# Kernel optimization log

Measured on AMD Instinct MI355X. Metric: run time of the kernel, lower is better.

## Reference

```python
import jax, jax.numpy as jnp
import numpy as np

D = 256; NH = 8; NL = 4; NP = 4; DH = D // NH; DFFN = 1024; NQ = 900; BS = 4
SPATIAL = ((92, 92), (46, 46), (23, 23), (12, 12))  # (H, W) per level
LEVEL_START = (0, 8464, 10580, 11109)
S = sum(h * w for h, w in SPATIAL)  # 11253


def _ln(x, g, b):
    m = jnp.mean(x, -1, keepdims=True)
    v = jnp.var(x, -1, keepdims=True)
    return (x - m) / jnp.sqrt(v + 1e-5) * g + b


def setup_inputs() -> dict:
    key = jax.random.key(0)
    ks = jax.random.split(key, 24)
    p = lambda k, s: 0.02 * jax.random.normal(k, s, jnp.float32)
    return {
        "tgt": jax.random.normal(ks[0], (NQ, BS, D), jnp.float32),
        "tgt_query_pos": jax.random.normal(ks[1], (NQ, BS, D), jnp.float32),
        "tgt_reference_points": jax.random.uniform(ks[2], (NQ, BS, NL, 2), jnp.float32),
        "memory": jax.random.normal(ks[3], (S, BS, D), jnp.float32),
        "memory_spatial_shapes": jnp.array(SPATIAL, jnp.int32),
        "memory_level_start_index": jnp.array(LEVEL_START, jnp.int32),
        "in_proj_w": p(ks[4], (3 * D, D)), "in_proj_b": p(ks[5], (3 * D,)),
        "out_proj_w": p(ks[6], (D, D)), "out_proj_b": p(ks[7], (D,)),
        "off_w": p(ks[8], (NH * NL * NP * 2, D)), "off_b": p(ks[9], (NH * NL * NP * 2,)),
        "aw_w": p(ks[10], (NH * NL * NP, D)), "aw_b": p(ks[11], (NH * NL * NP,)),
        "vproj_w": p(ks[12], (D, D)), "vproj_b": p(ks[13], (D,)),
        "oproj_w": p(ks[14], (D, D)), "oproj_b": p(ks[15], (D,)),
        "ln1_g": jnp.ones((D,), jnp.float32), "ln1_b": jnp.zeros((D,), jnp.float32),
        "ln2_g": jnp.ones((D,), jnp.float32), "ln2_b": jnp.zeros((D,), jnp.float32),
        "ln3_g": jnp.ones((D,), jnp.float32), "ln3_b": jnp.zeros((D,), jnp.float32),
        "lin1_w": p(ks[16], (DFFN, D)), "lin1_b": p(ks[17], (DFFN,)),
        "lin2_w": p(ks[18], (D, DFFN)), "lin2_b": p(ks[19], (D,)),
    }


def _self_attn(q, k, v, in_w, in_b, out_w, out_b):
    # q, k, v: (nq, bs, d) -- torch nn.MultiheadAttention, eval mode
    wq, wk, wv = jnp.split(in_w, 3, axis=0)
    bq, bk, bv = jnp.split(in_b, 3)
    qp = (q @ wq.T + bq).reshape(NQ, BS, NH, DH)
    kp = (k @ wk.T + bk).reshape(NQ, BS, NH, DH)
    vp = (v @ wv.T + bv).reshape(NQ, BS, NH, DH)
    s = jnp.einsum("qbhd,kbhd->bhqk", qp, kp) / jnp.sqrt(jnp.float32(DH))
    a = jax.nn.softmax(s, axis=-1)
    o = jnp.einsum("bhqk,kbhd->qbhd", a, vp).reshape(NQ, BS, D)
    return o @ out_w.T + out_b


def _msdeform(x, ref, mem, off_w, off_b, aw_w, aw_b, vproj_w, vproj_b, oproj_w, oproj_b):
    # x: (bs, nq, d); ref: (bs, nq, nl, 2) in [0,1]; mem: (bs, S, d)
    value = (mem @ vproj_w.T + vproj_b).reshape(BS, S, NH, DH)
    off = (x @ off_w.T + off_b).reshape(BS, NQ, NH, NL, NP, 2)
    aw = jax.nn.softmax((x @ aw_w.T + aw_b).reshape(BS, NQ, NH, NL * NP), axis=-1)
    aw = aw.reshape(BS, NQ, NH, NL, NP)
    # offset normalizer = (W, H) per level
    norm = jnp.array([[w, h] for (h, w) in SPATIAL], jnp.float32)
    loc = ref[:, :, None, :, None, :] + off / norm[None, None, None, :, None, :]
    out = jnp.zeros((BS, NH, NQ, DH), x.dtype)
    for l, (H, W) in enumerate(SPATIAL):
        s0 = LEVEL_START[l]
        v = value[:, s0:s0 + H * W].transpose(0, 2, 1, 3)  # (bs, nh, H*W, dh)
        g = loc[:, :, :, l].transpose(0, 2, 1, 3, 4)       # (bs, nh, nq, np, 2)
        # grid_sample align_corners=False, padding_mode='zeros'
        px = g[..., 0] * W - 0.5
        py = g[..., 1] * H - 0.5
        x0 = jnp.floor(px).astype(jnp.int32)
        y0 = jnp.floor(py).astype(jnp.int32)
        wx = px - x0
        wy = py - y0
        samp = jnp.zeros((BS, NH, NQ, NP, DH), x.dtype)
        for dx, dy, w in ((0, 0, (1 - wx) * (1 - wy)), (1, 0, wx * (1 - wy)),
                          (0, 1, (1 - wx) * wy), (1, 1, wx * wy)):
            xi = x0 + dx
            yi = y0 + dy
            valid = ((xi >= 0) & (xi < W) & (yi >= 0) & (yi < H)).astype(x.dtype)
            idx = (jnp.clip(yi, 0, H - 1) * W + jnp.clip(xi, 0, W - 1)).reshape(BS, NH, NQ * NP)
            gat = jnp.take_along_axis(v, idx[..., None], axis=2).reshape(BS, NH, NQ, NP, DH)
            samp = samp + (w * valid)[..., None] * gat
        a = aw[:, :, :, l].transpose(0, 2, 1, 3)  # (bs, nh, nq, np)
        out = out + (samp * a[..., None]).sum(axis=3)
    out = out.transpose(0, 2, 1, 3).reshape(BS, NQ, D)
    return out @ oproj_w.T + oproj_b


def reference(tgt, tgt_query_pos, tgt_reference_points, memory,
              memory_spatial_shapes, memory_level_start_index,
              in_proj_w, in_proj_b, out_proj_w, out_proj_b,
              off_w, off_b, aw_w, aw_b, vproj_w, vproj_b, oproj_w, oproj_b,
              ln1_g, ln1_b, ln2_g, ln2_b, ln3_g, ln3_b,
              lin1_w, lin1_b, lin2_w, lin2_b):
    # module_seq = ['sa', 'ca', 'ffn']; dropout inactive (eval)
    q = tgt + tgt_query_pos
    tgt2 = _self_attn(q, q, tgt, in_proj_w, in_proj_b, out_proj_w, out_proj_b)
    tgt = _ln(tgt + tgt2, ln2_g, ln2_b)
    x = (tgt + tgt_query_pos).transpose(1, 0, 2)
    ref = tgt_reference_points.transpose(1, 0, 2, 3)
    mem = memory.transpose(1, 0, 2)
    tgt2 = _msdeform(x, ref, mem, off_w, off_b, aw_w, aw_b,
                     vproj_w, vproj_b, oproj_w, oproj_b).transpose(1, 0, 2)
    tgt = _ln(tgt + tgt2, ln1_g, ln1_b)
    ff = jax.nn.relu(tgt @ lin1_w.T + lin1_b) @ lin2_w.T + lin2_b
    return _ln(tgt + ff, ln3_g, ln3_b)
```

## Files before the change

### kernel.cpp

```cpp
#include <hip/hip_runtime.h>
#include <math.h>

#define D_MODEL 256
#define NHEAD   8
#define NLVL    4
#define NPTS    4
#define DHEAD   32
#define DFFN    1024
#define NQ      900
#define BSZ     4
#define NROW    (NQ * BSZ)
#define S_TOT   11253
#define VROWS   (S_TOT * BSZ)
#define SASCALE 0.17677669529663687f

typedef __attribute__((ext_vector_type(8))) short short8;
typedef __attribute__((ext_vector_type(4))) float f32x4;
typedef unsigned short ushort_t;

static __device__ __forceinline__ unsigned f2bf1(float f) {
    unsigned u = __float_as_uint(f);
    return (u + 0x7FFFu + ((u >> 16) & 1u)) >> 16;
}
static __device__ __forceinline__ unsigned pack2bf(float x, float y) {
    return f2bf1(x) | (f2bf1(y) << 16);
}
static __device__ __forceinline__ float bf2f(ushort_t u) {
    return __uint_as_float(((unsigned)u) << 16);
}

#define GPAD 72

#if __has_builtin(__builtin_amdgcn_global_load_lds)
#define HAS_GLL 1
#endif

static __device__ __forceinline__ void stage_w16(const ushort_t* g, ushort_t* ldsbase, int lane)
{
#ifdef HAS_GLL
    __builtin_amdgcn_global_load_lds(
        (const __attribute__((address_space(1))) unsigned int*)g,
        (__attribute__((address_space(3))) unsigned int*)ldsbase, 16, 0, 0);
#else
    *(uint4*)(ldsbase + lane * 8) = *(const uint4*)g;
#endif
}

#define WB_IN   0
#define WB_VP   196608
#define WB_OUTP 262144
#define WB_OFF  327680
#define WB_AW   393216
#define WB_OP   425984
#define WB_L1   491520
#define WB_L2   753664
#define WB_TOT  1015808

__global__ __launch_bounds__(256) void cvt_weights(
    const float* __restrict__ w_in, const float* __restrict__ w_vp,
    const float* __restrict__ w_outp, const float* __restrict__ w_off,
    const float* __restrict__ w_aw, const float* __restrict__ w_op,
    const float* __restrict__ w_l1, const float* __restrict__ w_l2,
    ushort_t* __restrict__ dst)
{
    int b = blockIdx.x;
    const float* src;
    int dstoff;
    int kbits = 8;
    if (b < 96)       { src = w_in;   dstoff = WB_IN;   }
    else if (b < 128) { src = w_vp;   b -= 96;  dstoff = WB_VP;   }
    else if (b < 160) { src = w_outp; b -= 128; dstoff = WB_OUTP; }
    else if (b < 192) { src = w_off;  b -= 160; dstoff = WB_OFF;  }
    else if (b < 208) { src = w_aw;   b -= 192; dstoff = WB_AW;   }
    else if (b < 240) { src = w_op;   b -= 208; dstoff = WB_OP;   }
    else if (b < 368) { src = w_l1;   b -= 240; dstoff = WB_L1;   }
    else              { src = w_l2;   b -= 368; dstoff = WB_L2;   kbits = 10; }
    int i = (b * 256 + threadIdx.x) * 8;
    float4 f0 = *(const float4*)(src + i);
    float4 f1 = *(const float4*)(src + i + 4);
    uint4 u;
    u.x = pack2bf(f0.x, f0.y); u.y = pack2bf(f0.z, f0.w);
    u.z = pack2bf(f1.x, f1.y); u.w = pack2bf(f1.z, f1.w);
    int K = 1 << kbits;
    int n = i >> kbits;
    int k = i & (K - 1);
    int kswz = (k & ~63) | ((k & 63) ^ ((n & 7) << 3));
    *(uint4*)(dst + dstoff + (size_t)n * K + kswz) = u;
}

__global__ __launch_bounds__(256) void proj_fused(
    const float* __restrict__ tgt, const float* __restrict__ qpos,
    const ushort_t* __restrict__ in_wb, const float* __restrict__ in_b,
    const float* __restrict__ mem, const ushort_t* __restrict__ vp_wb,
    const float* __restrict__ vp_b,
    ushort_t* __restrict__ qkv16, ushort_t* __restrict__ value16)
{
    __shared__ ushort_t As[64 * GPAD];
    __shared__ ushort_t Ws[8704];

    const int t    = threadIdx.x;
    const int bid  = blockIdx.x;
    const int trow = t >> 2;
    const int tk   = (t & 3) << 4;
    const int wv   = t >> 6;
    const int ln   = t & 63;
    const int L    = ln & 15;
    const int quad = ln >> 4;
    const int swz  = (L & 7) << 3;
    const int lrow = ln >> 3;
    const int lchk = (ln & 7) << 3;

    if (bid < 684) {
        const int m0 = (bid % 57) * 64;
        const int n0 = (bid / 57) * 64;
        const bool addpos = (n0 < 512);
        const float oscale = (n0 < 256) ? SASCALE : 1.f;

        const int  mrow = m0 + trow;
        const bool mv   = (mrow < NROW);
        const float* arow = tgt  + (size_t)mrow * 256 + tk;
        const float* prow = qpos + (size_t)mrow * 256 + tk;

        f32x4 acc[4] = {{0.f,0.f,0.f,0.f},{0.f,0.f,0.f,0.f},
                        {0.f,0.f,0.f,0.f},{0.f,0.f,0.f,0.f}};

        for (int k0 = 0; k0 < 256; k0 += 64) {
#pragma unroll
            for (int j = 0; j < 2; ++j) {
                int r0 = (wv * 2 + j) * 8;
                const ushort_t* g = in_wb + (size_t)(n0 + r0 + lrow) * 256 + k0 + lchk;
                stage_w16(g, &Ws[r0 * 64], ln);
            }
            uint4 u0, u1;
            if (mv) {
                const float* ap = arow + k0;
                float4 a0 = *(const float4*)(ap + 0);
                float4 a1 = *(const float4*)(ap + 4);
                float4 a2 = *(const float4*)(ap + 8);
                float4 a3 = *(const float4*)(ap + 12);
                if (addpos) {
                    const float* pp = prow + k0;
                    float4 p0 = *(const float4*)(pp + 0);
                    float4 p1 = *(const float4*)(pp + 4);
                    float4 p2 = *(const float4*)(pp + 8);
                    float4 p3 = *(const float4*)(pp + 12);
                    a0.x += p0.x; a0.y += p0.y; a0.z += p0.z; a0.w += p0.w;
                    a1.x += p1.x; a1.y += p1.y; a1.z += p1.z; a1.w += p1.w;
                    a2.x += p2.x; a2.y += p2.y; a2.z += p2.z; a2.w += p2.w;
                    a3.x += p3.x; a3.y += p3.y; a3.z += p3.z; a3.w += p3.w;
                }
                u0.x = pack2bf(a0.x, a0.y); u0.y = pack2bf(a0.z, a0.w);
                u0.z = pack2bf(a1.x, a1.y); u0.w = pack2bf(a1.z, a1.w);
                u1.x = pack2bf(a2.x, a2.y); u1.y = pack2bf(a2.z, a2.w);
                u1.z = pack2bf(a3.x, a3.y); u1.w = pack2bf(a3.z, a3.w);
            } else {
                u0 = make_uint4(0u, 0u, 0u, 0u); u1 = u0;
            }
            *(uint4*)&As[trow * GPAD + tk + 0] = u0;
            *(uint4*)&As[trow * GPAD + tk + 8] = u1;
            __syncthreads();
#pragma unroll
            for (int kh = 0; kh < 2; ++kh) {
                short8 af = *(const short8*)&As[(wv * 16 + L) * GPAD + kh * 32 + quad * 8];
#pragma unroll
                for (int cb = 0; cb < 4; ++cb) {
                    short8 bf = *(const short8*)&Ws[(cb * 16 + L) * 64 + ((kh * 32 + quad * 8) ^ swz)];
                    acc[cb] = __builtin_amdgcn_mfma_f32_16x16x32_bf16(af, bf, acc[cb], 0, 0, 0);
                }
            }
            __syncthreads();
        }
#pragma unroll
        for (int cb = 0; cb < 4; ++cb) {
            int col = n0 + cb * 16 + L;
            float bv = in_b[col];
#pragma unroll
            for (int i = 0; i < 4; ++i) {
                int m = m0 + wv * 16 + quad * 4 + i;
                if (m < NROW)
                    qkv16[(size_t)m * 768 + col] = (ushort_t)f2bf1((acc[cb][i] + bv) * oscale);
            }
        }
    } else {
        const int vb = bid - 684;
        const int m0 = vb * 64;

        const int  mrow = m0 + trow;
        const bool mv   = (mrow < VROWS);
        const float* arow = mem + (size_t)mrow * 256 + tk;

        f32x4 acc[16];
#pragma unroll
        for (int i = 0; i < 16; ++i) acc[i] = (f32x4){0.f, 0.f, 0.f, 0.f};

        for (int k0 = 0; k0 < 256; k0 += 64) {
#pragma unroll
            for (int j = 0; j < 4; ++j) {
                int r0 = (wv * 4 + j) * 8;
                const ushort_t* g = vp_wb + (size_t)(r0 + lrow) * 256 + k0 + lchk;
                stage_w16(g, &Ws[r0 * 64], ln);
            }
            uint4 u0, u1;
            if (mv) {
                const float* ap = arow + k0;
                float4 a0 = *(const float4*)(ap + 0);
                float4 a1 = *(const float4*)(ap + 4);
                float4 a2 = *(const float4*)(ap + 8);
                float4 a3 = *(const float4*)(ap + 12);
                u0.x = pack2bf(a0.x, a0.y); u0.y = pack2bf(a0.z, a0.w);
                u0.z = pack2bf(a1.x, a1.y); u0.w = pack2bf(a1.z, a1.w);
                u1.x = pack2bf(a2.x, a2.y); u1.y = pack2bf(a2.z, a2.w);
                u1.z = pack2bf(a3.x, a3.y); u1.w = pack2bf(a3.z, a3.w);
            } else {
                u0 = make_uint4(0u, 0u, 0u, 0u); u1 = u0;
            }
            *(uint4*)&As[trow * GPAD + tk + 0] = u0;
            *(uint4*)&As[trow * GPAD + tk + 8] = u1;
            __syncthreads();
#pragma unroll
            for (int kh = 0; kh < 2; ++kh) {
                short8 af = *(const short8*)&As[(wv * 16 + L) * GPAD + kh * 32 + quad * 8];
#pragma unroll
                for (int cb = 0; cb < 8; ++cb) {
                    short8 bf = *(const short8*)&Ws[(cb * 16 + L) * 64 + ((kh * 32 + quad * 8) ^ swz)];
                    acc[cb] = __builtin_amdgcn_mfma_f32_16x16x32_bf16(af, bf, acc[cb], 0, 0, 0);
                }
            }
            __syncthreads();
#pragma unroll
            for (int j = 0; j < 4; ++j) {
                int r0 = (wv * 4 + j) * 8;
                const ushort_t* g = vp_wb + (size_t)(128 + r0 + lrow) * 256 + k0 + lchk;
                stage_w16(g, &Ws[r0 * 64], ln);
            }
            __syncthreads();
#pragma unroll
            for (int kh = 0; kh < 2; ++kh) {
                short8 af = *(const short8*)&As[(wv * 16 + L) * GPAD + kh * 32 + quad * 8];
#pragma unroll
                for (int cb = 0; cb < 8; ++cb) {
                    short8 bf = *(const short8*)&Ws[(cb * 16 + L) * 64 + ((kh * 32 + quad * 8) ^ swz)];
                    acc[8 + cb] = __builtin_amdgcn_mfma_f32_16x16x32_bf16(af, bf, acc[8 + cb], 0, 0, 0);
                }
            }
            __syncthreads();
        }

        ushort_t* Cs = Ws;
#pragma unroll
        for (int half = 0; half < 2; ++half) {
            if (half) __syncthreads();
#pragma unroll
            for (int cb = 0; cb < 8; ++cb) {
                int col = cb * 16 + L;
                float bv = vp_b[half * 128 + col];
#pragma unroll
                for (int i = 0; i < 4; ++i) {
                    int r = wv * 16 + quad * 4 + i;
                    Cs[r * 136 + col] = (ushort_t)f2bf1(acc[half * 8 + cb][i] + bv);
                }
            }
            __syncthreads();
            {
                int r  = t >> 2;
                int ch = (t & 3) * 32;
                int m  = m0 + r;
                if (m < VROWS) {
                    const ushort_t* src = &Cs[r * 136 + ch];
                    uint4* dst = (uint4*)(value16 + (size_t)m * 256 + half * 128 + ch);
#pragma unroll
                    for (int j = 0; j < 4; ++j)
                        dst[j] = *(const uint4*)(src + j * 8);
                }
            }
        }
    }
}

__global__ __launch_bounds__(256) void sa_flash16(
    const ushort_t* __restrict__ qkv, ushort_t* __restrict__ attn_out)
{
    __shared__ ushort_t Ks[2 * 2080];
    __shared__ ushort_t Vt[2 * 2304];
    __shared__ ushort_t Ps[4 * 1152];

    const int t    = threadIdx.x;
    const int q0   = blockIdx.x * 64;
    const int b    = blockIdx.y & 3;
    const int h    = blockIdx.y >> 2;
    const int wv   = t >> 6;
    const int ln   = t & 63;
    const int L    = ln & 15;
    const int quad = ln >> 4;

    union { uint4 u; short8 s; } qu;
    qu.u = make_uint4(0u, 0u, 0u, 0u);
    {
        int q = q0 + wv * 16 + L;
        if (q < NQ)
            qu.u = *(const uint4*)(qkv + ((size_t)q * 4 + b) * 768 + h * 32 + quad * 8);
    }
    const short8 qf = qu.s;

    float mrun = -1e30f, lrun = 0.f;
    f32x4 oacc[2] = {{0.f,0.f,0.f,0.f},{0.f,0.f,0.f,0.f}};

    const int skey = t >> 2;
    const int sdg  = t & 3;

    uint4 ku, vu;
    auto kv_load = [&](int k0) {
        int kg = k0 + skey;
        ku = make_uint4(0u, 0u, 0u, 0u);
        vu = make_uint4(0u, 0u, 0u, 0u);
        if (kg < NQ) {
            const ushort_t* base = qkv + ((size_t)kg * 4 + b) * 768 + 256 + h * 32 + sdg * 8;
            ku = *(const uint4*)base;
            vu = *(const uint4*)(base + 256);
        }
    };

    kv_load(0);
    int it = 0;
    for (int k0 = 0; k0 < NQ; k0 += 64, it ^= 1) {
        *(uint4*)&Ks[it * 2080 + sdg * 520 + skey * 8] = ku;
        {
            ushort_t* vp = &Vt[it * 2304 + sdg * 8 * 72 + skey];
            vp[0 * 72] = (ushort_t)(vu.x & 0xffffu);
            vp[1 * 72] = (ushort_t)(vu.x >> 16);
            vp[2 * 72] = (ushort_t)(vu.y & 0xffffu);
            vp[3 * 72] = (ushort_t)(vu.y >> 16);
            vp[4 * 72] = (ushort_t)(vu.z & 0xffffu);
            vp[5 * 72] = (ushort_t)(vu.z >> 16);
            vp[6 * 72] = (ushort_t)(vu.w & 0xffffu);
            vp[7 * 72] = (ushort_t)(vu.w >> 16);
        }
        __syncthreads();
        if (k0 + 64 < NQ) kv_load(k0 + 64);

        f32x4 sacc[4] = {{0.f,0.f,0.f,0.f},{0.f,0.f,0.f,0.f},
                         {0.f,0.f,0.f,0.f},{0.f,0.f,0.f,0.f}};
#pragma unroll
        for (int cb = 0; cb < 4; ++cb) {
            short8 kf = *(const short8*)&Ks[it * 2080 + quad * 520 + (cb * 16 + L) * 8];
            sacc[cb] = __builtin_amdgcn_mfma_f32_16x16x32_bf16(kf, qf, sacc[cb], 0, 0, 0);
        }
        if (k0 + 64 > NQ) {
#pragma unroll
            for (int cb = 0; cb < 4; ++cb)
#pragma unroll
                for (int i = 0; i < 4; ++i)
                    if (k0 + cb * 16 + quad * 4 + i >= NQ) sacc[cb][i] = -1e30f;
        }

        float ml = -1e30f;
#pragma unroll
        for (int cb = 0; cb < 4; ++cb)
#pragma unroll
            for (int i = 0; i < 4; ++i) ml = fmaxf(ml, sacc[cb][i]);
        ml = fmaxf(ml, __shfl_xor(ml, 16, 64));
        ml = fmaxf(ml, __shfl_xor(ml, 32, 64));
        float mnew  = fmaxf(mrun, ml);
        float alpha = __expf(mrun - mnew);
        float p[16];
        float rs = 0.f;
#pragma unroll
        for (int cb = 0; cb < 4; ++cb)
#pragma unroll
            for (int i = 0; i < 4; ++i) {
                float e = __expf(sacc[cb][i] - mnew);
                p[cb * 4 + i] = e;
                rs += e;
            }
        rs += __shfl_xor(rs, 16, 64);
        rs += __shfl_xor(rs, 32, 64);
        lrun = lrun * alpha + rs;
        mrun = mnew;

        {
            ushort_t* pw = &Ps[wv * 1152 + L * 72];
#pragma unroll
            for (int cb = 0; cb < 4; ++cb) {
                uint2 u;
                u.x = pack2bf(p[cb * 4 + 0], p[cb * 4 + 1]);
                u.y = pack2bf(p[cb * 4 + 2], p[cb * 4 + 3]);
                *(uint2*)&pw[cb * 16 + quad * 4] = u;
            }
        }
#pragma unroll
        for (int i = 0; i < 4; ++i) {
            float ai = __shfl(alpha, quad * 4 + i, 64);
            oacc[0][i] *= ai;
            oacc[1][i] *= ai;
        }
        __syncthreads();

#pragma unroll
        for (int ks = 0; ks < 2; ++ks) {
            short8 pf = *(const short8*)&Ps[wv * 1152 + L * 72 + ks * 32 + quad * 8];
#pragma unroll
            for (int db = 0; db < 2; ++db) {
                short8 vf = *(const short8*)&Vt[it * 2304 + (db * 16 + L) * 72 + ks * 32 + quad * 8];
                oacc[db] = __builtin_amdgcn_mfma_f32_16x16x32_bf16(pf, vf, oacc[db], 0, 0, 0);
            }
        }
    }

#pragma unroll
    for (int i = 0; i < 4; ++i) {
        float lq = __shfl(lrun, quad * 4 + i, 64);
        float li = 1.f / lq;
        int q = q0 + wv * 16 + quad * 4 + i;
        if (q < NQ) {
            ushort_t* op = attn_out + ((size_t)q * 4 + b) * 256 + h * 32 + L;
            op[0]  = (ushort_t)f2bf1(oacc[0][i] * li);
            op[16] = (ushort_t)f2bf1(oacc[1][i] * li);
        }
    }
}

__global__ __launch_bounds__(256) void fused_ca(
    const ushort_t* __restrict__ att16,
    const float* __restrict__ tgt, const float* __restrict__ qpos,
    const ushort_t* __restrict__ outp_wb, const float* __restrict__ outp_b,
    const float* __restrict__ ln2g, const float* __restrict__ ln2b,
    const ushort_t* __restrict__ off_wb, const float* __restrict__ off_b,
    const ushort_t* __restrict__ aw_wb, const float* __restrict__ aw_b,
    const float* __restrict__ refp,
    float* __restrict__ tgt_a, float* __restrict__ px_g,
    float* __restrict__ py_g, float* __restrict__ aw_g)
{
    __shared__ ushort_t Ws[256 * 64];
    __shared__ ushort_t As[16 * GPAD];
    __shared__ ushort_t xca_s[16 * 264];
    __shared__ float    aws[16 * 128];
    __shared__ float    sS[4][16], s2S[4][16];

    const int t    = threadIdx.x;
    const int m0   = blockIdx.x * 16;
    const int wv   = t >> 6;
    const int ln   = t & 63;
    const int L    = ln & 15;
    const int quad = ln >> 4;
    const int swz  = (L & 7) << 3;
    const int lrow = ln >> 3;
    const int lchk = (ln & 7) << 3;
    const int rloc = quad * 4;

    {
        f32x4 acc[4] = {{0.f,0.f,0.f,0.f},{0.f,0.f,0.f,0.f},
                        {0.f,0.f,0.f,0.f},{0.f,0.f,0.f,0.f}};
        for (int k0 = 0; k0 < 256; k0 += 64) {
#pragma unroll
            for (int j = 0; j < 8; ++j) {
                int r0 = (wv * 8 + j) * 8;
                const ushort_t* g = outp_wb + (size_t)(r0 + lrow) * 256 + k0 + lchk;
                stage_w16(g, &Ws[r0 * 64], ln);
            }
            if (t < 128) {
                int r = t >> 3, seg = (t & 7) * 8;
                uint4 a = *(const uint4*)(att16 + (size_t)(m0 + r) * 256 + k0 + seg);
                *(uint4*)&As[r * GPAD + seg] = a;
            }
            __syncthreads();
#pragma unroll
            for (int kh = 0; kh < 2; ++kh) {
                short8 af = *(const short8*)&As[L * GPAD + kh * 32 + quad * 8];
#pragma unroll
                for (int cb = 0; cb < 4; ++cb) {
                    short8 bf = *(const short8*)&Ws[(wv * 64 + cb * 16 + L) * 64 + ((kh * 32 + quad * 8) ^ swz)];
                    acc[cb] = __builtin_amdgcn_mfma_f32_16x16x32_bf16(af, bf, acc[cb], 0, 0, 0);
                }
            }
            __syncthreads();
        }
        float s[4] = {0.f,0.f,0.f,0.f}, s2v[4] = {0.f,0.f,0.f,0.f};
#pragma unroll
        for (int cb = 0; cb < 4; ++cb) {
            int col = wv * 64 + cb * 16 + L;
            float bv = outp_b[col];
#pragma unroll
            for (int i = 0; i < 4; ++i) {
                float xv = acc[cb][i] + bv + tgt[(size_t)(m0 + rloc + i) * 256 + col];
                acc[cb][i] = xv;
                s[i] += xv; s2v[i] += xv * xv;
            }
        }
#pragma unroll
        for (int off = 1; off < 16; off <<= 1)
#pragma unroll
            for (int i = 0; i < 4; ++i) {
                s[i]   += __shfl_xor(s[i],   off, 64);
                s2v[i] += __shfl_xor(s2v[i], off, 64);
            }
        if (L == 0)
#pragma unroll
            for (int i = 0; i < 4; ++i) { sS[wv][rloc + i] = s[i]; s2S[wv][rloc + i] = s2v[i]; }
        __syncthreads();
        float mean[4], rstd[4];
#pragma unroll
        for (int i = 0; i < 4; ++i) {
            float St  = sS[0][rloc+i] + sS[1][rloc+i] + sS[2][rloc+i] + sS[3][rloc+i];
            float S2t = s2S[0][rloc+i] + s2S[1][rloc+i] + s2S[2][rloc+i] + s2S[3][rloc+i];
            mean[i] = St * (1.f / 256.f);
            float var = S2t * (1.f / 256.f) - mean[i] * mean[i];
            rstd[i] = rsqrtf(var + 1e-5f);
        }
#pragma unroll
        for (int cb = 0; cb < 4; ++cb) {
            int col = wv * 64 + cb * 16 + L;
            float gv = ln2g[col], bt = ln2b[col];
#pragma unroll
            for (int i = 0; i < 4; ++i) {
                float y = (acc[cb][i] - mean[i]) * rstd[i] * gv + bt;
                tgt_a[(size_t)(m0 + rloc + i) * 256 + col] = y;
                xca_s[(rloc + i) * 264 + col] =
                    (ushort_t)f2bf1(y + qpos[(size_t)(m0 + rloc + i) * 256 + col]);
            }
        }
        __syncthreads();
    }

    {
        f32x4 acc[4] = {{0.f,0.f,0.f,0.f},{0.f,0.f,0.f,0.f},
                        {0.f,0.f,0.f,0.f},{0.f,0.f,0.f,0.f}};
        for (int k0 = 0; k0 < 256; k0 += 64) {
#pragma unroll
            for (int j = 0; j < 8; ++j) {
                int r0 = (wv * 8 + j) * 8;
                const ushort_t* g = off_wb + (size_t)(r0 + lrow) * 256 + k0 + lchk;
                stage_w16(g, &Ws[r0 * 64], ln);
            }
            __syncthreads();
#pragma unroll
            for (int kh = 0; kh < 2; ++kh) {
                short8 af = *(const short8*)&xca_s[L * 264 + k0 + kh * 32 + quad * 8];
#pragma unroll
                for (int cb = 0; cb < 4; ++cb) {
                    short8 bf = *(const short8*)&Ws[(wv * 64 + cb * 16 + L) * 64 + ((kh * 32 + quad * 8) ^ swz)];
                    acc[cb] = __builtin_amdgcn_mfma_f32_16x16x32_bf16(af, bf, acc[cb], 0, 0, 0);
                }
            }
            __syncthreads();
        }
        const float dims[4] = {92.f, 46.f, 23.f, 12.f};
#pragma unroll
        for (int cb = 0; cb < 4; ++cb) {
            int col = wv * 64 + cb * 16 + L;
            float bv = off_b[col];
            int hh = col >> 5, lp = (col & 31) >> 1, isY = col & 1;
            int l = lp >> 2;
            float dim = dims[l];
            float* dst = isY ? py_g : px_g;
#pragma unroll
            for (int i = 0; i < 4; ++i) {
                int row = m0 + rloc + i;
                float ref = refp[((size_t)row * 4 + l) * 2 + isY];
                dst[(size_t)row * 128 + hh * 16 + lp] = ref * dim + (acc[cb][i] + bv) - 0.5f;
            }
        }
    }

    {
        f32x4 acc2[2] = {{0.f,0.f,0.f,0.f},{0.f,0.f,0.f,0.f}};
        for (int k0 = 0; k0 < 256; k0 += 64) {
#pragma unroll
            for (int j = 0; j < 4; ++j) {
                int r0 = (wv * 4 + j) * 8;
                const ushort_t* g = aw_wb + (size_t)(r0 + lrow) * 256 + k0 + lchk;
                stage_w16(g, &Ws[r0 * 64], ln);
            }
            __syncthreads();
#pragma unroll
            for (int kh = 0; kh < 2; ++kh) {
                short8 af = *(const short8*)&xca_s[L * 264 + k0 + kh * 32 + quad * 8];
#pragma unroll
                for (int cb = 0; cb < 2; ++cb) {
                    short8 bf = *(const short8*)&Ws[(wv * 32 + cb * 16 + L) * 64 + ((kh * 32 + quad * 8) ^ swz)];
                    acc2[cb] = __builtin_amdgcn_mfma_f32_16x16x32_bf16(af, bf, acc2[cb], 0, 0, 0);
                }
            }
            __syncthreads();
        }
#pragma unroll
        for (int cb = 0; cb < 2; ++cb) {
            int col = wv * 32 + cb * 16 + L;
            float bv = aw_b[col];
#pragma unroll
            for (int i = 0; i < 4; ++i)
                aws[(rloc + i) * 128 + col] = acc2[cb][i] + bv;
        }
        __syncthreads();
    }

    if (t < 128) {
        int r = t >> 3, hh = t & 7;
        float v[16];
        float m = -1e30f;
#pragma unroll
        for (int j = 0; j < 16; ++j) { v[j] = aws[r * 128 + hh * 16 + j]; m = fmaxf(m, v[j]); }
        float ssum = 0.f;
#pragma unroll
        for (int j = 0; j < 16; ++j) { v[j] = __expf(v[j] - m); ssum += v[j]; }
        float inv = 1.f / ssum;
#pragma unroll
        for (int j = 0; j < 16; ++j)
            aw_g[(size_t)(m0 + r) * 128 + hh * 16 + j] = v[j] * inv;
    }
}

__global__ __launch_bounds__(256) void msdeform4(
    const float* __restrict__ px_g, const float* __restrict__ py_g,
    const float* __restrict__ aw_g, const ushort_t* __restrict__ value16,
    ushort_t* __restrict__ out)
{
    const int t   = threadIdx.x;
    const int row = blockIdx.x * 4 + (t >> 6);
    const int ln  = t & 63;
    const int h   = ln >> 3;
    const int d   = (ln & 7) * 4;
    const int b   = row & 3;

    const int HsI[4] = {92, 46, 23, 12};
    const int S0_[4] = {0, 8464, 10580, 11109};

    const ushort_t* vb = value16 + (size_t)b * 256 + h * 32 + d;
    const float* pxr = px_g + (size_t)row * 128 + h * 16;
    const float* pyr = py_g + (size_t)row * 128 + h * 16;
    const float* awr = aw_g + (size_t)row * 128 + h * 16;

    float a0 = 0.f, a1 = 0.f, a2 = 0.f, a3 = 0.f;
#pragma unroll
    for (int l = 0; l < 4; ++l) {
        const int H = HsI[l], W = HsI[l], base = S0_[l];
#pragma unroll
        for (int p = 0; p < 4; ++p) {
            const int lp = l * 4 + p;
            float px = pxr[lp], py = pyr[lp], aw = awr[lp];
            float x0f = floorf(px), y0f = floorf(py);
            int x0 = (int)x0f, y0 = (int)y0f;
            float wx = px - x0f, wy = py - y0f;
            float s0 = 0.f, s1 = 0.f, s2 = 0.f, s3 = 0.f;
#pragma unroll
            for (int dy = 0; dy < 2; ++dy) {
#pragma unroll
                for (int dx = 0; dx < 2; ++dx) {
                    int xi = x0 + dx, yi = y0 + dy;
                    float flag = (xi >= 0 && xi < W && yi >= 0 && yi < H) ? 1.f : 0.f;
                    int xc = xi < 0 ? 0 : (xi >= W ? W - 1 : xi);
                    int yc = yi < 0 ? 0 : (yi >= H ? H - 1 : yi);
                    float wgt = (dx ? wx : 1.f - wx) * (dy ? wy : 1.f - wy) * flag;
                    uint2 gv = *(const uint2*)(vb + (size_t)(base + yc * W + xc) * 1024);
                    s0 = fmaf(wgt, bf2f((ushort_t)(gv.x & 0xffffu)), s0);
                    s1 = fmaf(wgt, bf2f((ushort_t)(gv.x >> 16)), s1);
                    s2 = fmaf(wgt, bf2f((ushort_t)(gv.y & 0xffffu)), s2);
                    s3 = fmaf(wgt, bf2f((ushort_t)(gv.y >> 16)), s3);
                }
            }
            a0 = fmaf(aw, s0, a0);
            a1 = fmaf(aw, s1, a1);
            a2 = fmaf(aw, s2, a2);
            a3 = fmaf(aw, s3, a3);
        }
    }
    uint2 u;
    u.x = pack2bf(a0, a1);
    u.y = pack2bf(a2, a3);
    *(uint2*)(out + (size_t)row * 256 + h * 32 + d) = u;
}

__global__ __launch_bounds__(256) void ffn_fused(
    const ushort_t* __restrict__ att2_16,
    const float* __restrict__ tgt_a,
    const ushort_t* __restrict__ op_wb, const float* __restrict__ op_b,
    const float* __restrict__ ln1g, const float* __restrict__ ln1b,
    const ushort_t* __restrict__ l1_wb, const float* __restrict__ l1b,
    const ushort_t* __restrict__ l2_wb, const float* __restrict__ l2b,
    const float* __restrict__ ln3g, const float* __restrict__ ln3b,
    float* __restrict__ out)
{
    __shared__ ushort_t Ws[256 * 64];
    __shared__ ushort_t A1[16 * 264];
    __shared__ ushort_t hc[16 * 264];
    __shared__ float    sS[4][16], s2S[4][16];

    const int t    = threadIdx.x;
    const int m0   = blockIdx.x * 16;
    const int wv   = t >> 6;
    const int ln   = t & 63;
    const int L    = ln & 15;
    const int quad = ln >> 4;
    const int swz  = (L & 7) << 3;
    const int lrow = ln >> 3;
    const int lchk = (ln & 7) << 3;
    const int rloc = quad * 4;

#pragma unroll
    for (int jj = 0; jj < 2; ++jj) {
        int c = t * 2 + jj;
        int r = c >> 5, s = (c & 31) * 8;
        *(uint4*)&hc[r * 264 + s] = *(const uint4*)(att2_16 + (size_t)(m0 + r) * 256 + s);
    }

    f32x4 resid[4];

    {
        f32x4 acc[4] = {{0.f,0.f,0.f,0.f},{0.f,0.f,0.f,0.f},
                        {0.f,0.f,0.f,0.f},{0.f,0.f,0.f,0.f}};
        for (int k0 = 0; k0 < 256; k0 += 64) {
#pragma unroll
            for (int j = 0; j < 8; ++j) {
                int r0 = (wv * 8 + j) * 8;
                const ushort_t* g = op_wb + (size_t)(r0 + lrow) * 256 + k0 + lchk;
                stage_w16(g, &Ws[r0 * 64], ln);
            }
            __syncthreads();
#pragma unroll
            for (int kh = 0; kh < 2; ++kh) {
                short8 af = *(const short8*)&hc[L * 264 + k0 + kh * 32 + quad * 8];
#pragma unroll
                for (int cb = 0; cb < 4; ++cb) {
                    short8 bf = *(const short8*)&Ws[(wv * 64 + cb * 16 + L) * 64 + ((kh * 32 + quad * 8) ^ swz)];
                    acc[cb] = __builtin_amdgcn_mfma_f32_16x16x32_bf16(af, bf, acc[cb], 0, 0, 0);
                }
            }
            __syncthreads();
        }
        float s[4] = {0.f,0.f,0.f,0.f}, s2v[4] = {0.f,0.f,0.f,0.f};
#pragma unroll
        for (int cb = 0; cb < 4; ++cb) {
            int col = wv * 64 + cb * 16 + L;
            float bv = op_b[col];
#pragma unroll
            for (int i = 0; i < 4; ++i) {
                float xv = acc[cb][i] + bv + tgt_a[(size_t)(m0 + rloc + i) * 256 + col];
                acc[cb][i] = xv;
                s[i] += xv; s2v[i] += xv * xv;
            }
        }
#pragma unroll
        for (int off = 1; off < 16; off <<= 1)
#pragma unroll
            for (int i = 0; i < 4; ++i) {
                s[i]   += __shfl_xor(s[i],   off, 64);
                s2v[i] += __shfl_xor(s2v[i], off, 64);
            }
        if (L == 0)
#pragma unroll
            for (int i = 0; i < 4; ++i) { sS[wv][rloc + i] = s[i]; s2S[wv][rloc + i] = s2v[i]; }
        __syncthreads();
        float mean[4], rstd[4];
#pragma unroll
        for (int i = 0; i < 4; ++i) {
            float St  = sS[0][rloc+i] + sS[1][rloc+i] + sS[2][rloc+i] + sS[3][rloc+i];
            float S2t = s2S[0][rloc+i] + s2S[1][rloc+i] + s2S[2][rloc+i] + s2S[3][rloc+i];
            mean[i] = St * (1.f / 256.f);
            float var = S2t * (1.f / 256.f) - mean[i] * mean[i];
            rstd[i] = rsqrtf(var + 1e-5f);
        }
#pragma unroll
        for (int cb = 0; cb < 4; ++cb) {
            int col = wv * 64 + cb * 16 + L;
            float gv = ln1g[col], bt = ln1b[col];
#pragma unroll
            for (int i = 0; i < 4; ++i) {
                float y = (acc[cb][i] - mean[i]) * rstd[i] * gv + bt;
                resid[cb][i] = y;
                A1[(rloc + i) * 264 + col] = (ushort_t)f2bf1(y);
            }
        }
        __syncthreads();
    }

    f32x4 accf[4] = {{0.f,0.f,0.f,0.f},{0.f,0.f,0.f,0.f},
                     {0.f,0.f,0.f,0.f},{0.f,0.f,0.f,0.f}};
    for (int c = 0; c < 4; ++c) {
        f32x4 acch[4] = {{0.f,0.f,0.f,0.f},{0.f,0.f,0.f,0.f},
                         {0.f,0.f,0.f,0.f},{0.f,0.f,0.f,0.f}};
        for (int k0 = 0; k0 < 256; k0 += 64) {
#pragma unroll
            for (int j = 0; j < 8; ++j) {
                int r0 = (wv * 8 + j) * 8;
                const ushort_t* g = l1_wb + (size_t)(c * 256 + r0 + lrow) * 256 + k0 + lchk;
                stage_w16(g, &Ws[r0 * 64], ln);
            }
            __syncthreads();
#pragma unroll
            for (int kh = 0; kh < 2; ++kh) {
                short8 af = *(const short8*)&A1[L * 264 + k0 + kh * 32 + quad * 8];
#pragma unroll
                for (int cb = 0; cb < 4; ++cb) {
                    short8 bf = *(const short8*)&Ws[(wv * 64 + cb * 16 + L) * 64 + ((kh * 32 + quad * 8) ^ swz)];
                    acch[cb] = __builtin_amdgcn_mfma_f32_16x16x32_bf16(af, bf, acch[cb], 0, 0, 0);
                }
            }
            __syncthreads();
        }
#pragma unroll
        for (int cb = 0; cb < 4; ++cb) {
            int colc = wv * 64 + cb * 16 + L;
            float bv = l1b[c * 256 + colc];
#pragma unroll
            for (int i = 0; i < 4; ++i)
                hc[(rloc + i) * 264 + colc] = (ushort_t)f2bf1(fmaxf(acch[cb][i] + bv, 0.f));
        }
        __syncthreads();
        for (int k0 = 0; k0 < 256; k0 += 64) {
#pragma unroll
            for (int j = 0; j < 8; ++j) {
                int r0 = (wv * 8 + j) * 8;
                const ushort_t* g = l2_wb + (size_t)(r0 + lrow) * 1024 + c * 256 + k0 + lchk;
                stage_w16(g, &Ws[r0 * 64], ln);
            }
            __syncthreads();
#pragma unroll
            for (int kh = 0; kh < 2; ++kh) {
                short8 af = *(const short8*)&hc[L * 264 + k0 + kh * 32 + quad * 8];
#pragma unroll
                for (int cb = 0; cb < 4; ++cb) {
                    short8 bf = *(const short8*)&Ws[(wv * 64 + cb * 16 + L) * 64 + ((kh * 32 + quad * 8) ^ swz)];
                    accf[cb] = __builtin_amdgcn_mfma_f32_16x16x32_bf16(af, bf, accf[cb], 0, 0, 0);
                }
            }
            __syncthreads();
        }
    }

    {
        float s[4] = {0.f,0.f,0.f,0.f}, s2v[4] = {0.f,0.f,0.f,0.f};
#pragma unroll
        for (int cb = 0; cb < 4; ++cb) {
            int col = wv * 64 + cb * 16 + L;
            float bv = l2b[col];
#pragma unroll
            for (int i = 0; i < 4; ++i) {
                float xv = accf[cb][i] + bv + resid[cb][i];
                accf[cb][i] = xv;
                s[i] += xv; s2v[i] += xv * xv;
            }
        }
#pragma unroll
        for (int off = 1; off < 16; off <<= 1)
#pragma unroll
            for (int i = 0; i < 4; ++i) {
                s[i]   += __shfl_xor(s[i],   off, 64);
                s2v[i] += __shfl_xor(s2v[i], off, 64);
            }
        if (L == 0)
#pragma unroll
            for (int i = 0; i < 4; ++i) { sS[wv][rloc + i] = s[i]; s2S[wv][rloc + i] = s2v[i]; }
        __syncthreads();
        float mean[4], rstd[4];
#pragma unroll
        for (int i = 0; i < 4; ++i) {
            float St  = sS[0][rloc+i] + sS[1][rloc+i] + sS[2][rloc+i] + sS[3][rloc+i];
            float S2t = s2S[0][rloc+i] + s2S[1][rloc+i] + s2S[2][rloc+i] + s2S[3][rloc+i];
            mean[i] = St * (1.f / 256.f);
            float var = S2t * (1.f / 256.f) - mean[i] * mean[i];
            rstd[i] = rsqrtf(var + 1e-5f);
        }
#pragma unroll
        for (int cb = 0; cb < 4; ++cb) {
            int col = wv * 64 + cb * 16 + L;
            float gv = ln3g[col], bt = ln3b[col];
#pragma unroll
            for (int i = 0; i < 4; ++i) {
                float y = (accf[cb][i] - mean[i]) * rstd[i] * gv + bt;
                out[(size_t)(m0 + rloc + i) * 256 + col] = y;
            }
        }
    }
}

extern "C" void kernel_launch(void* const* d_in, const int* in_sizes, int n_in,
                              void* d_out, int out_size, void* d_ws, size_t ws_size,
                              hipStream_t stream)
{
    const float* tgt    = (const float*)d_in[0];
    const float* qpos   = (const float*)d_in[1];
    const float* refp   = (const float*)d_in[2];
    const float* mem    = (const float*)d_in[3];
    const float* in_w   = (const float*)d_in[6];
    const float* in_b   = (const float*)d_in[7];
    const float* outp_w = (const float*)d_in[8];
    const float* outp_b = (const float*)d_in[9];
    const float* off_w  = (const float*)d_in[10];
    const float* off_b  = (const float*)d_in[11];
    const float* aw_w   = (const float*)d_in[12];
    const float* aw_b   = (const float*)d_in[13];
    const float* vp_w   = (const float*)d_in[14];
    const float* vp_b   = (const float*)d_in[15];
    const float* op_w   = (const float*)d_in[16];
    const float* op_b   = (const float*)d_in[17];
    const float* ln1g   = (const float*)d_in[18];
    const float* ln1b   = (const float*)d_in[19];
    const float* ln2g   = (const float*)d_in[20];
    const float* ln2b   = (const float*)d_in[21];
    const float* ln3g   = (const float*)d_in[22];
    const float* ln3b   = (const float*)d_in[23];
    const float* l1w    = (const float*)d_in[24];
    const float* l1b    = (const float*)d_in[25];
    const float* l2w    = (const float*)d_in[26];
    const float* l2b    = (const float*)d_in[27];
    float* out = (float*)d_out;
    float* ws  = (float*)d_ws;

    ushort_t* qkv16    = (ushort_t*)ws;
    ushort_t* att16    = (ushort_t*)(ws + 691200);
    float*    tgt_a    = ws + 1843200;
    float*    px_g     = ws + 2995200;
    float*    py_g     = ws + 3456000;
    float*    aw_g     = ws + 3916800;
    ushort_t* att2_16  = (ushort_t*)(ws + 4377600);
    ushort_t* value16  = (ushort_t*)(ws + 5760000);
    ushort_t* wb       = (ushort_t*)(ws + 13364736);

    const ushort_t* in_wb   = wb + WB_IN;
    const ushort_t* vp_wb   = wb + WB_VP;
    const ushort_t* outp_wb = wb + WB_OUTP;
    const ushort_t* off_wb  = wb + WB_OFF;
    const ushort_t* aw_wb   = wb + WB_AW;
    const ushort_t* op_wb   = wb + WB_OP;
    const ushort_t* l1_wb   = wb + WB_L1;
    const ushort_t* l2_wb   = wb + WB_L2;

    dim3 b256(256);

    hipLaunchKernelGGL(cvt_weights, dim3(496), b256, 0, stream,
                       in_w, vp_w, outp_w, off_w, aw_w, op_w, l1w, l2w, wb);
    hipLaunchKernelGGL(proj_fused, dim3(1388), b256, 0, stream,
                       tgt, qpos, in_wb, in_b, mem, vp_wb, vp_b, qkv16, value16);
    hipLaunchKernelGGL(sa_flash16, dim3(15, 32), b256, 0, stream, qkv16, att16);
    hipLaunchKernelGGL(fused_ca, dim3(225), b256, 0, stream,
                       att16, tgt, qpos, outp_wb, outp_b, ln2g, ln2b,
                       off_wb, off_b, aw_wb, aw_b, refp,
                       tgt_a, px_g, py_g, aw_g);
    hipLaunchKernelGGL(msdeform4, dim3(900), b256, 0, stream,
                       px_g, py_g, aw_g, value16, att2_16);
    hipLaunchKernelGGL(ffn_fused, dim3(225), b256, 0, stream,
                       att2_16, tgt_a, op_wb, op_b, ln1g, ln1b,
                       l1_wb, l1b, l2_wb, l2b, ln3g, ln3b, out);
}
```

Baseline: 255.2 us.

## Pre-convert activations to bf16, double-buffer weights, widen fused kernels to 512 threads

The weight-conversion kernel now also converts tgt and tgt+qpos into swizzled bf16 buffers, so the QKV projection can stage its A tiles directly with global_load_lds instead of converting fp32 per tile. The value projection stages all 256 weight rows at once, removing a second staging pass and one barrier per k-step. fused_ca and ffn_fused move to 512 threads with double-buffered weight tiles in LDS, prefetching the next k-slice or the next GEMM's first slice while the current one computes, which halves the barriers per step. The cost is extra workspace traffic for the bf16 activation copies, more LDS per block, and a single resident block per CU for the fused kernels.

```diff
diff --git a/kernel.cpp b/kernel.cpp
--- a/kernel.cpp
+++ b/kernel.cpp
@@ -10,6 +10,7 @@
 #define NQ      900
 #define BSZ     4
 #define NROW    (NQ * BSZ)
+#define NROWP   3648
 #define S_TOT   11253
 #define VROWS   (S_TOT * BSZ)
 #define SASCALE 0.17677669529663687f
@@ -28,8 +29,6 @@
 static __device__ __forceinline__ float bf2f(ushort_t u) {
     return __uint_as_float(((unsigned)u) << 16);
 }
-
-#define GPAD 72
 
 #if __has_builtin(__builtin_amdgcn_global_load_lds)
 #define HAS_GLL 1
@@ -61,47 +60,73 @@
     const float* __restrict__ w_outp, const float* __restrict__ w_off,
     const float* __restrict__ w_aw, const float* __restrict__ w_op,
     const float* __restrict__ w_l1, const float* __restrict__ w_l2,
-    ushort_t* __restrict__ dst)
+    ushort_t* __restrict__ dst,
+    const float* __restrict__ tgt, const float* __restrict__ qpos,
+    ushort_t* __restrict__ tgt16, ushort_t* __restrict__ tq16)
 {
     int b = blockIdx.x;
-    const float* src;
-    int dstoff;
-    int kbits = 8;
-    if (b < 96)       { src = w_in;   dstoff = WB_IN;   }
-    else if (b < 128) { src = w_vp;   b -= 96;  dstoff = WB_VP;   }
-    else if (b < 160) { src = w_outp; b -= 128; dstoff = WB_OUTP; }
-    else if (b < 192) { src = w_off;  b -= 160; dstoff = WB_OFF;  }
-    else if (b < 208) { src = w_aw;   b -= 192; dstoff = WB_AW;   }
-    else if (b < 240) { src = w_op;   b -= 208; dstoff = WB_OP;   }
-    else if (b < 368) { src = w_l1;   b -= 240; dstoff = WB_L1;   }
-    else              { src = w_l2;   b -= 368; dstoff = WB_L2;   kbits = 10; }
-    int i = (b * 256 + threadIdx.x) * 8;
-    float4 f0 = *(const float4*)(src + i);
-    float4 f1 = *(const float4*)(src + i + 4);
-    uint4 u;
-    u.x = pack2bf(f0.x, f0.y); u.y = pack2bf(f0.z, f0.w);
-    u.z = pack2bf(f1.x, f1.y); u.w = pack2bf(f1.z, f1.w);
-    int K = 1 << kbits;
-    int n = i >> kbits;
-    int k = i & (K - 1);
-    int kswz = (k & ~63) | ((k & 63) ^ ((n & 7) << 3));
-    *(uint4*)(dst + dstoff + (size_t)n * K + kswz) = u;
+    if (b < 496) {
+        const float* src;
+        int dstoff;
+        int kbits = 8;
+        if (b < 96)       { src = w_in;   dstoff = WB_IN;   }
+        else if (b < 128) { src = w_vp;   b -= 96;  dstoff = WB_VP;   }
+        else if (b < 160) { src = w_outp; b -= 128; dstoff = WB_OUTP; }
+        else if (b < 192) { src = w_off;  b -= 160; dstoff = WB_OFF;  }
+        else if (b < 208) { src = w_aw;   b -= 192; dstoff = WB_AW;   }
+        else if (b < 240) { src = w_op;   b -= 208; dstoff = WB_OP;   }
+        else if (b < 368) { src = w_l1;   b -= 240; dstoff = WB_L1;   }
+        else              { src = w_l2;   b -= 368; dstoff = WB_L2;   kbits = 10; }
+        int i = (b * 256 + threadIdx.x) * 8;
+        float4 f0 = *(const float4*)(src + i);
+        float4 f1 = *(const float4*)(src + i + 4);
+        uint4 u;
+        u.x = pack2bf(f0.x, f0.y); u.y = pack2bf(f0.z, f0.w);
+        u.z = pack2bf(f1.x, f1.y); u.w = pack2bf(f1.z, f1.w);
+        int K = 1 << kbits;
+        int n = i >> kbits;
+        int k = i & (K - 1);
+        int kswz = (k & ~63) | ((k & 63) ^ ((n & 7) << 3));
+        *(uint4*)(dst + dstoff + (size_t)n * K + kswz) = u;
+    } else {
+        int bb = b - 496;
+        ushort_t* dbuf = tgt16;
+        bool addq = false;
+        if (bb >= 456) { bb -= 456; dbuf = tq16; addq = true; }
+        int i = bb * 2048 + threadIdx.x * 8;
+        int row = i >> 8, k = i & 255;
+        uint4 u = make_uint4(0u, 0u, 0u, 0u);
+        if (row < NROW) {
+            const float* sp = tgt + (size_t)row * 256 + k;
+            float4 f0 = *(const float4*)(sp + 0);
+            float4 f1 = *(const float4*)(sp + 4);
+            if (addq) {
+                const float* qp = qpos + (size_t)row * 256 + k;
+                float4 q0 = *(const float4*)(qp + 0);
+                float4 q1 = *(const float4*)(qp + 4);
+                f0.x += q0.x; f0.y += q0.y; f0.z += q0.z; f0.w += q0.w;
+                f1.x += q1.x; f1.y += q1.y; f1.z += q1.z; f1.w += q1.w;
+            }
+            u.x = pack2bf(f0.x, f0.y); u.y = pack2bf(f0.z, f0.w);
+            u.z = pack2bf(f1.x, f1.y); u.w = pack2bf(f1.z, f1.w);
+        }
+        int kswz = (k & ~63) | ((k & 63) ^ ((row & 7) << 3));
+        *(uint4*)(dbuf + (size_t)row * 256 + kswz) = u;
+    }
 }
 
 __global__ __launch_bounds__(256) void proj_fused(
-    const float* __restrict__ tgt, const float* __restrict__ qpos,
+    const ushort_t* __restrict__ tq16, const ushort_t* __restrict__ tgt16,
     const ushort_t* __restrict__ in_wb, const float* __restrict__ in_b,
     const float* __restrict__ mem, const ushort_t* __restrict__ vp_wb,
     const float* __restrict__ vp_b,
     ushort_t* __restrict__ qkv16, ushort_t* __restrict__ value16)
 {
-    __shared__ ushort_t As[64 * GPAD];
-    __shared__ ushort_t Ws[8704];
+    __shared__ ushort_t As[64 * 64];
+    __shared__ ushort_t Ws[256 * 64];
 
     const int t    = threadIdx.x;
     const int bid  = blockIdx.x;
-    const int trow = t >> 2;
-    const int tk   = (t & 3) << 4;
     const int wv   = t >> 6;
     const int ln   = t & 63;
     const int L    = ln & 15;
@@ -113,13 +138,8 @@
     if (bid < 684) {
         const int m0 = (bid % 57) * 64;
         const int n0 = (bid / 57) * 64;
-        const bool addpos = (n0 < 512);
         const float oscale = (n0 < 256) ? SASCALE : 1.f;
-
-        const int  mrow = m0 + trow;
-        const bool mv   = (mrow < NROW);
-        const float* arow = tgt  + (size_t)mrow * 256 + tk;
-        const float* prow = qpos + (size_t)mrow * 256 + tk;
+        const ushort_t* Ab = (n0 < 512) ? tq16 : tgt16;
 
         f32x4 acc[4] = {{0.f,0.f,0.f,0.f},{0.f,0.f,0.f,0.f},
                         {0.f,0.f,0.f,0.f},{0.f,0.f,0.f,0.f}};
@@ -128,43 +148,17 @@
 #pragma unroll
             for (int j = 0; j < 2; ++j) {
                 int r0 = (wv * 2 + j) * 8;
-                const ushort_t* g = in_wb + (size_t)(n0 + r0 + lrow) * 256 + k0 + lchk;
-                stage_w16(g, &Ws[r0 * 64], ln);
-            }
-            uint4 u0, u1;
-            if (mv) {
-                const float* ap = arow + k0;
-                float4 a0 = *(const float4*)(ap + 0);
-                float4 a1 = *(const float4*)(ap + 4);
-                float4 a2 = *(const float4*)(ap + 8);
-                float4 a3 = *(const float4*)(ap + 12);
-                if (addpos) {
-                    const float* pp = prow + k0;
-                    float4 p0 = *(const float4*)(pp + 0);
-                    float4 p1 = *(const float4*)(pp + 4);
-                    float4 p2 = *(const float4*)(pp + 8);
-                    float4 p3 = *(const float4*)(pp + 12);
-                    a0.x += p0.x; a0.y += p0.y; a0.z += p0.z; a0.w += p0.w;
-                    a1.x += p1.x; a1.y += p1.y; a1.z += p1.z; a1.w += p1.w;
-                    a2.x += p2.x; a2.y += p2.y; a2.z += p2.z; a2.w += p2.w;
-                    a3.x += p3.x; a3.y += p3.y; a3.z += p3.z; a3.w += p3.w;
-                }
-                u0.x = pack2bf(a0.x, a0.y); u0.y = pack2bf(a0.z, a0.w);
-                u0.z = pack2bf(a1.x, a1.y); u0.w = pack2bf(a1.z, a1.w);
-                u1.x = pack2bf(a2.x, a2.y); u1.y = pack2bf(a2.z, a2.w);
-                u1.z = pack2bf(a3.x, a3.y); u1.w = pack2bf(a3.z, a3.w);
-            } else {
-                u0 = make_uint4(0u, 0u, 0u, 0u); u1 = u0;
-            }
-            *(uint4*)&As[trow * GPAD + tk + 0] = u0;
-            *(uint4*)&As[trow * GPAD + tk + 8] = u1;
+                stage_w16(Ab + (size_t)(m0 + r0 + lrow) * 256 + k0 + lchk, &As[r0 * 64], ln);
+                stage_w16(in_wb + (size_t)(n0 + r0 + lrow) * 256 + k0 + lchk, &Ws[r0 * 64], ln);
+            }
             __syncthreads();
 #pragma unroll
             for (int kh = 0; kh < 2; ++kh) {
-                short8 af = *(const short8*)&As[(wv * 16 + L) * GPAD + kh * 32 + quad * 8];
+                int ko = (kh * 32 + quad * 8) ^ swz;
+                short8 af = *(const short8*)&As[(wv * 16 + L) * 64 + ko];
 #pragma unroll
                 for (int cb = 0; cb < 4; ++cb) {
-                    short8 bf = *(const short8*)&Ws[(cb * 16 + L) * 64 + ((kh * 32 + quad * 8) ^ swz)];
+                    short8 bf = *(const short8*)&Ws[(cb * 16 + L) * 64 + ko];
                     acc[cb] = __builtin_amdgcn_mfma_f32_16x16x32_bf16(af, bf, acc[cb], 0, 0, 0);
                 }
             }
@@ -184,6 +178,9 @@
     } else {
         const int vb = bid - 684;
         const int m0 = vb * 64;
+        const int trow = t >> 2;
+        const int tk   = (t & 3) << 4;
+        const int wsz  = (trow & 7) << 3;
 
         const int  mrow = m0 + trow;
         const bool mv   = (mrow < VROWS);
@@ -195,10 +192,9 @@
 
         for (int k0 = 0; k0 < 256; k0 += 64) {
 #pragma unroll
-            for (int j = 0; j < 4; ++j) {
-                int r0 = (wv * 4 + j) * 8;
-                const ushort_t* g = vp_wb + (size_t)(r0 + lrow) * 256 + k0 + lchk;
-                stage_w16(g, &Ws[r0 * 64], ln);
+            for (int j = 0; j < 8; ++j) {
+                int r0 = (wv * 8 + j) * 8;
+                stage_w16(vp_wb + (size_t)(r0 + lrow) * 256 + k0 + lchk, &Ws[r0 * 64], ln);
             }
             uint4 u0, u1;
             if (mv) {
@@ -214,33 +210,17 @@
             } else {
                 u0 = make_uint4(0u, 0u, 0u, 0u); u1 = u0;
             }
-            *(uint4*)&As[trow * GPAD + tk + 0] = u0;
-            *(uint4*)&As[trow * GPAD + tk + 8] = u1;
+            *(uint4*)&As[trow * 64 + (tk ^ wsz)]       = u0;
+            *(uint4*)&As[trow * 64 + ((tk + 8) ^ wsz)] = u1;
             __syncthreads();
 #pragma unroll
             for (int kh = 0; kh < 2; ++kh) {
-                short8 af = *(const short8*)&As[(wv * 16 + L) * GPAD + kh * 32 + quad * 8];
-#pragma unroll
-                for (int cb = 0; cb < 8; ++cb) {
-                    short8 bf = *(const short8*)&Ws[(cb * 16 + L) * 64 + ((kh * 32 + quad * 8) ^ swz)];
+                int ko = (kh * 32 + quad * 8) ^ swz;
+                short8 af = *(const short8*)&As[(wv * 16 + L) * 64 + ko];
+#pragma unroll
+                for (int cb = 0; cb < 16; ++cb) {
+                    short8 bf = *(const short8*)&Ws[(cb * 16 + L) * 64 + ko];
                     acc[cb] = __builtin_amdgcn_mfma_f32_16x16x32_bf16(af, bf, acc[cb], 0, 0, 0);
-                }
-            }
-            __syncthreads();
-#pragma unroll
-            for (int j = 0; j < 4; ++j) {
-                int r0 = (wv * 4 + j) * 8;
-                const ushort_t* g = vp_wb + (size_t)(128 + r0 + lrow) * 256 + k0 + lchk;
-                stage_w16(g, &Ws[r0 * 64], ln);
-            }
-            __syncthreads();
-#pragma unroll
-            for (int kh = 0; kh < 2; ++kh) {
-                short8 af = *(const short8*)&As[(wv * 16 + L) * GPAD + kh * 32 + quad * 8];
-#pragma unroll
-                for (int cb = 0; cb < 8; ++cb) {
-                    short8 bf = *(const short8*)&Ws[(cb * 16 + L) * 64 + ((kh * 32 + quad * 8) ^ swz)];
-                    acc[8 + cb] = __builtin_amdgcn_mfma_f32_16x16x32_bf16(af, bf, acc[8 + cb], 0, 0, 0);
                 }
             }
             __syncthreads();
@@ -419,7 +399,7 @@
     }
 }
 
-__global__ __launch_bounds__(256) void fused_ca(
+__global__ __launch_bounds__(512, 1) void fused_ca(
     const ushort_t* __restrict__ att16,
     const float* __restrict__ tgt, const float* __restrict__ qpos,
     const ushort_t* __restrict__ outp_wb, const float* __restrict__ outp_b,
@@ -430,11 +410,11 @@
     float* __restrict__ tgt_a, float* __restrict__ px_g,
     float* __restrict__ py_g, float* __restrict__ aw_g)
 {
-    __shared__ ushort_t Ws[256 * 64];
-    __shared__ ushort_t As[16 * GPAD];
+    __shared__ ushort_t Ws[2][256 * 64];
+    __shared__ ushort_t att_s[16 * 264];
     __shared__ ushort_t xca_s[16 * 264];
-    __shared__ float    aws[16 * 128];
-    __shared__ float    sS[4][16], s2S[4][16];
+    __shared__ float    aws_s[16 * 128];
+    __shared__ float    sS[8][16], s2S[8][16];
 
     const int t    = threadIdx.x;
     const int m0   = blockIdx.x * 16;
@@ -447,37 +427,54 @@
     const int lchk = (ln & 7) << 3;
     const int rloc = quad * 4;
 
+    auto stage4 = [&](const ushort_t* base, int buf) {
+#pragma unroll
+        for (int j = 0; j < 4; ++j) {
+            int r0 = (wv * 4 + j) * 8;
+            stage_w16(base + (size_t)(r0 + lrow) * 256 + lchk, &Ws[buf][r0 * 64], ln);
+        }
+    };
+    auto stage2 = [&](const ushort_t* base, int buf) {
+#pragma unroll
+        for (int j = 0; j < 2; ++j) {
+            int r0 = (wv * 2 + j) * 8;
+            stage_w16(base + (size_t)(r0 + lrow) * 256 + lchk, &Ws[buf][r0 * 64], ln);
+        }
+    };
+    auto mfma2 = [&](const ushort_t* A, int koff, int buf, f32x4* acc) {
+#pragma unroll
+        for (int kh = 0; kh < 2; ++kh) {
+            int ko = (kh * 32 + quad * 8) ^ swz;
+            short8 af = *(const short8*)&A[L * 264 + koff + kh * 32 + quad * 8];
+#pragma unroll
+            for (int cb = 0; cb < 2; ++cb) {
+                short8 bf = *(const short8*)&Ws[buf][(wv * 32 + cb * 16 + L) * 64 + ko];
+                acc[cb] = __builtin_amdgcn_mfma_f32_16x16x32_bf16(af, bf, acc[cb], 0, 0, 0);
+            }
+        }
+    };
+
     {
-        f32x4 acc[4] = {{0.f,0.f,0.f,0.f},{0.f,0.f,0.f,0.f},
-                        {0.f,0.f,0.f,0.f},{0.f,0.f,0.f,0.f}};
-        for (int k0 = 0; k0 < 256; k0 += 64) {
-#pragma unroll
-            for (int j = 0; j < 8; ++j) {
-                int r0 = (wv * 8 + j) * 8;
-                const ushort_t* g = outp_wb + (size_t)(r0 + lrow) * 256 + k0 + lchk;
-                stage_w16(g, &Ws[r0 * 64], ln);
-            }
-            if (t < 128) {
-                int r = t >> 3, seg = (t & 7) * 8;
-                uint4 a = *(const uint4*)(att16 + (size_t)(m0 + r) * 256 + k0 + seg);
-                *(uint4*)&As[r * GPAD + seg] = a;
-            }
-            __syncthreads();
-#pragma unroll
-            for (int kh = 0; kh < 2; ++kh) {
-                short8 af = *(const short8*)&As[L * GPAD + kh * 32 + quad * 8];
-#pragma unroll
-                for (int cb = 0; cb < 4; ++cb) {
-                    short8 bf = *(const short8*)&Ws[(wv * 64 + cb * 16 + L) * 64 + ((kh * 32 + quad * 8) ^ swz)];
-                    acc[cb] = __builtin_amdgcn_mfma_f32_16x16x32_bf16(af, bf, acc[cb], 0, 0, 0);
-                }
-            }
-            __syncthreads();
+        int r = t >> 5, s = (t & 31) * 8;
+        *(uint4*)&att_s[r * 264 + s] = *(const uint4*)(att16 + (size_t)(m0 + r) * 256 + s);
+    }
+    stage4(outp_wb, 0);
+    __syncthreads();
+    int cur = 0;
+
+    {
+        f32x4 acc[2] = {{0.f,0.f,0.f,0.f},{0.f,0.f,0.f,0.f}};
+        for (int k = 0; k < 4; ++k) {
+            if (k < 3) stage4(outp_wb + (k + 1) * 64, cur ^ 1);
+            else       stage4(off_wb, cur ^ 1);
+            mfma2(att_s, k * 64, cur, acc);
+            __syncthreads();
+            cur ^= 1;
         }
         float s[4] = {0.f,0.f,0.f,0.f}, s2v[4] = {0.f,0.f,0.f,0.f};
 #pragma unroll
-        for (int cb = 0; cb < 4; ++cb) {
-            int col = wv * 64 + cb * 16 + L;
+        for (int cb = 0; cb < 2; ++cb) {
+            int col = wv * 32 + cb * 16 + L;
             float bv = outp_b[col];
 #pragma unroll
             for (int i = 0; i < 4; ++i) {
@@ -500,15 +497,16 @@
         float mean[4], rstd[4];
 #pragma unroll
         for (int i = 0; i < 4; ++i) {
-            float St  = sS[0][rloc+i] + sS[1][rloc+i] + sS[2][rloc+i] + sS[3][rloc+i];
-            float S2t = s2S[0][rloc+i] + s2S[1][rloc+i] + s2S[2][rloc+i] + s2S[3][rloc+i];
+            float St = 0.f, S2t = 0.f;
+#pragma unroll
+            for (int w = 0; w < 8; ++w) { St += sS[w][rloc + i]; S2t += s2S[w][rloc + i]; }
             mean[i] = St * (1.f / 256.f);
             float var = S2t * (1.f / 256.f) - mean[i] * mean[i];
             rstd[i] = rsqrtf(var + 1e-5f);
         }
 #pragma unroll
-        for (int cb = 0; cb < 4; ++cb) {
-            int col = wv * 64 + cb * 16 + L;
+        for (int cb = 0; cb < 2; ++cb) {
+            int col = wv * 32 + cb * 16 + L;
             float gv = ln2g[col], bt = ln2b[col];
 #pragma unroll
             for (int i = 0; i < 4; ++i) {
@@ -522,31 +520,18 @@
     }
 
     {
-        f32x4 acc[4] = {{0.f,0.f,0.f,0.f},{0.f,0.f,0.f,0.f},
-                        {0.f,0.f,0.f,0.f},{0.f,0.f,0.f,0.f}};
-        for (int k0 = 0; k0 < 256; k0 += 64) {
-#pragma unroll
-            for (int j = 0; j < 8; ++j) {
-                int r0 = (wv * 8 + j) * 8;
-                const ushort_t* g = off_wb + (size_t)(r0 + lrow) * 256 + k0 + lchk;
-                stage_w16(g, &Ws[r0 * 64], ln);
-            }
-            __syncthreads();
-#pragma unroll
-            for (int kh = 0; kh < 2; ++kh) {
-                short8 af = *(const short8*)&xca_s[L * 264 + k0 + kh * 32 + quad * 8];
-#pragma unroll
-                for (int cb = 0; cb < 4; ++cb) {
-                    short8 bf = *(const short8*)&Ws[(wv * 64 + cb * 16 + L) * 64 + ((kh * 32 + quad * 8) ^ swz)];
-                    acc[cb] = __builtin_amdgcn_mfma_f32_16x16x32_bf16(af, bf, acc[cb], 0, 0, 0);
-                }
-            }
-            __syncthreads();
+        f32x4 acc[2] = {{0.f,0.f,0.f,0.f},{0.f,0.f,0.f,0.f}};
+        for (int k = 0; k < 4; ++k) {
+            if (k < 3) stage4(off_wb + (k + 1) * 64, cur ^ 1);
+            else       stage2(aw_wb, cur ^ 1);
+            mfma2(xca_s, k * 64, cur, acc);
+            __syncthreads();
+            cur ^= 1;
         }
         const float dims[4] = {92.f, 46.f, 23.f, 12.f};
 #pragma unroll
-        for (int cb = 0; cb < 4; ++cb) {
-            int col = wv * 64 + cb * 16 + L;
+        for (int cb = 0; cb < 2; ++cb) {
+            int col = wv * 32 + cb * 16 + L;
             float bv = off_b[col];
             int hh = col >> 5, lp = (col & 31) >> 1, isY = col & 1;
             int l = lp >> 2;
@@ -562,33 +547,25 @@
     }
 
     {
-        f32x4 acc2[2] = {{0.f,0.f,0.f,0.f},{0.f,0.f,0.f,0.f}};
-        for (int k0 = 0; k0 < 256; k0 += 64) {
-#pragma unroll
-            for (int j = 0; j < 4; ++j) {
-                int r0 = (wv * 4 + j) * 8;
-                const ushort_t* g = aw_wb + (size_t)(r0 + lrow) * 256 + k0 + lchk;
-                stage_w16(g, &Ws[r0 * 64], ln);
-            }
-            __syncthreads();
+        f32x4 acc = {0.f, 0.f, 0.f, 0.f};
+        for (int k = 0; k < 4; ++k) {
+            if (k < 3) stage2(aw_wb + (k + 1) * 64, cur ^ 1);
 #pragma unroll
             for (int kh = 0; kh < 2; ++kh) {
-                short8 af = *(const short8*)&xca_s[L * 264 + k0 + kh * 32 + quad * 8];
-#pragma unroll
-                for (int cb = 0; cb < 2; ++cb) {
-                    short8 bf = *(const short8*)&Ws[(wv * 32 + cb * 16 + L) * 64 + ((kh * 32 + quad * 8) ^ swz)];
-                    acc2[cb] = __builtin_amdgcn_mfma_f32_16x16x32_bf16(af, bf, acc2[cb], 0, 0, 0);
-                }
-            }
-            __syncthreads();
-        }
-#pragma unroll
-        for (int cb = 0; cb < 2; ++cb) {
-            int col = wv * 32 + cb * 16 + L;
+                int ko = (kh * 32 + quad * 8) ^ swz;
+                short8 af = *(const short8*)&xca_s[L * 264 + k * 64 + kh * 32 + quad * 8];
+                short8 bf = *(const short8*)&Ws[cur][(wv * 16 + L) * 64 + ko];
+                acc = __builtin_amdgcn_mfma_f32_16x16x32_bf16(af, bf, acc, 0, 0, 0);
+            }
+            __syncthreads();
+            cur ^= 1;
+        }
+        {
+            int col = wv * 16 + L;
             float bv = aw_b[col];
 #pragma unroll
             for (int i = 0; i < 4; ++i)
-                aws[(rloc + i) * 128 + col] = acc2[cb][i] + bv;
+                aws_s[(rloc + i) * 128 + col] = acc[i] + bv;
         }
         __syncthreads();
     }
@@ -598,7 +575,7 @@
         float v[16];
         float m = -1e30f;
 #pragma unroll
-        for (int j = 0; j < 16; ++j) { v[j] = aws[r * 128 + hh * 16 + j]; m = fmaxf(m, v[j]); }
+        for (int j = 0; j < 16; ++j) { v[j] = aws_s[r * 128 + hh * 16 + j]; m = fmaxf(m, v[j]); }
         float ssum = 0.f;
 #pragma unroll
         for (int j = 0; j < 16; ++j) { v[j] = __expf(v[j] - m); ssum += v[j]; }
@@ -669,7 +646,7 @@
     *(uint2*)(out + (size_t)row * 256 + h * 32 + d) = u;
 }
 
-__global__ __launch_bounds__(256) void ffn_fused(
+__global__ __launch_bounds__(512, 1) void ffn_fused(
     const ushort_t* __restrict__ att2_16,
     const float* __restrict__ tgt_a,
     const ushort_t* __restrict__ op_wb, const float* __restrict__ op_b,
@@ -679,10 +656,10 @@
     const float* __restrict__ ln3g, const float* __restrict__ ln3b,
     float* __restrict__ out)
 {
-    __shared__ ushort_t Ws[256 * 64];
+    __shared__ ushort_t Ws[2][256 * 64];
     __shared__ ushort_t A1[16 * 264];
     __shared__ ushort_t hc[16 * 264];
-    __shared__ float    sS[4][16], s2S[4][16];
+    __shared__ float    sS[8][16], s2S[8][16];
 
     const int t    = threadIdx.x;
     const int m0   = blockIdx.x * 16;
@@ -695,41 +672,49 @@
     const int lchk = (ln & 7) << 3;
     const int rloc = quad * 4;
 
-#pragma unroll
-    for (int jj = 0; jj < 2; ++jj) {
-        int c = t * 2 + jj;
-        int r = c >> 5, s = (c & 31) * 8;
+    auto stageWs = [&](const ushort_t* base, int stride, int buf) {
+#pragma unroll
+        for (int j = 0; j < 4; ++j) {
+            int r0 = (wv * 4 + j) * 8;
+            stage_w16(base + (size_t)(r0 + lrow) * stride + lchk, &Ws[buf][r0 * 64], ln);
+        }
+    };
+    auto mfma2 = [&](const ushort_t* A, int koff, int buf, f32x4* acc) {
+#pragma unroll
+        for (int kh = 0; kh < 2; ++kh) {
+            int ko = (kh * 32 + quad * 8) ^ swz;
+            short8 af = *(const short8*)&A[L * 264 + koff + kh * 32 + quad * 8];
+#pragma unroll
+            for (int cb = 0; cb < 2; ++cb) {
+                short8 bf = *(const short8*)&Ws[buf][(wv * 32 + cb * 16 + L) * 64 + ko];
+                acc[cb] = __builtin_amdgcn_mfma_f32_16x16x32_bf16(af, bf, acc[cb], 0, 0, 0);
+            }
+        }
+    };
+
+    {
+        int r = t >> 5, s = (t & 31) * 8;
         *(uint4*)&hc[r * 264 + s] = *(const uint4*)(att2_16 + (size_t)(m0 + r) * 256 + s);
     }
-
-    f32x4 resid[4];
+    stageWs(op_wb, 256, 0);
+    __syncthreads();
+    int cur = 0;
+
+    f32x4 resid[2];
 
     {
-        f32x4 acc[4] = {{0.f,0.f,0.f,0.f},{0.f,0.f,0.f,0.f},
-                        {0.f,0.f,0.f,0.f},{0.f,0.f,0.f,0.f}};
-        for (int k0 = 0; k0 < 256; k0 += 64) {
-#pragma unroll
-            for (int j = 0; j < 8; ++j) {
-                int r0 = (wv * 8 + j) * 8;
-                const ushort_t* g = op_wb + (size_t)(r0 + lrow) * 256 + k0 + lchk;
-                stage_w16(g, &Ws[r0 * 64], ln);
-            }
-            __syncthreads();
-#pragma unroll
-            for (int kh = 0; kh < 2; ++kh) {
-                short8 af = *(const short8*)&hc[L * 264 + k0 + kh * 32 + quad * 8];
-#pragma unroll
-                for (int cb = 0; cb < 4; ++cb) {
-                    short8 bf = *(const short8*)&Ws[(wv * 64 + cb * 16 + L) * 64 + ((kh * 32 + quad * 8) ^ swz)];
-                    acc[cb] = __builtin_amdgcn_mfma_f32_16x16x32_bf16(af, bf, acc[cb], 0, 0, 0);
-                }
-            }
-            __syncthreads();
+        f32x4 acc[2] = {{0.f,0.f,0.f,0.f},{0.f,0.f,0.f,0.f}};
+        for (int k = 0; k < 4; ++k) {
+            if (k < 3) stageWs(op_wb + (k + 1) * 64, 256, cur ^ 1);
+            else       stageWs(l1_wb, 256, cur ^ 1);
+            mfma2(hc, k * 64, cur, acc);
+            __syncthreads();
+            cur ^= 1;
         }
         float s[4] = {0.f,0.f,0.f,0.f}, s2v[4] = {0.f,0.f,0.f,0.f};
 #pragma unroll
-        for (int cb = 0; cb < 4; ++cb) {
-            int col = wv * 64 + cb * 16 + L;
+        for (int cb = 0; cb < 2; ++cb) {
+            int col = wv * 32 + cb * 16 + L;
             float bv = op_b[col];
 #pragma unroll
             for (int i = 0; i < 4; ++i) {
@@ -752,15 +737,16 @@
         float mean[4], rstd[4];
 #pragma unroll
         for (int i = 0; i < 4; ++i) {
-            float St  = sS[0][rloc+i] + sS[1][rloc+i] + sS[2][rloc+i] + sS[3][rloc+i];
-            float S2t = s2S[0][rloc+i] + s2S[1][rloc+i] + s2S[2][rloc+i] + s2S[3][rloc+i];
+            float St = 0.f, S2t = 0.f;
+#pragma unroll
+            for (int w = 0; w < 8; ++w) { St += sS[w][rloc + i]; S2t += s2S[w][rloc + i]; }
             mean[i] = St * (1.f / 256.f);
             float var = S2t * (1.f / 256.f) - mean[i] * mean[i];
             rstd[i] = rsqrtf(var + 1e-5f);
         }
 #pragma unroll
-        for (int cb = 0; cb < 4; ++cb) {
-            int col = wv * 64 + cb * 16 + L;
+        for (int cb = 0; cb < 2; ++cb) {
+            int col = wv * 32 + cb * 16 + L;
             float gv = ln1g[col], bt = ln1b[col];
 #pragma unroll
             for (int i = 0; i < 4; ++i) {
@@ -772,65 +758,39 @@
         __syncthreads();
     }
 
-    f32x4 accf[4] = {{0.f,0.f,0.f,0.f},{0.f,0.f,0.f,0.f},
-                     {0.f,0.f,0.f,0.f},{0.f,0.f,0.f,0.f}};
+    f32x4 accf[2] = {{0.f,0.f,0.f,0.f},{0.f,0.f,0.f,0.f}};
     for (int c = 0; c < 4; ++c) {
-        f32x4 acch[4] = {{0.f,0.f,0.f,0.f},{0.f,0.f,0.f,0.f},
-                         {0.f,0.f,0.f,0.f},{0.f,0.f,0.f,0.f}};
-        for (int k0 = 0; k0 < 256; k0 += 64) {
-#pragma unroll
-            for (int j = 0; j < 8; ++j) {
-                int r0 = (wv * 8 + j) * 8;
-                const ushort_t* g = l1_wb + (size_t)(c * 256 + r0 + lrow) * 256 + k0 + lchk;
-                stage_w16(g, &Ws[r0 * 64], ln);
-            }
-            __syncthreads();
-#pragma unroll
-            for (int kh = 0; kh < 2; ++kh) {
-                short8 af = *(const short8*)&A1[L * 264 + k0 + kh * 32 + quad * 8];
-#pragma unroll
-                for (int cb = 0; cb < 4; ++cb) {
-                    short8 bf = *(const short8*)&Ws[(wv * 64 + cb * 16 + L) * 64 + ((kh * 32 + quad * 8) ^ swz)];
-                    acch[cb] = __builtin_amdgcn_mfma_f32_16x16x32_bf16(af, bf, acch[cb], 0, 0, 0);
-                }
-            }
-            __syncthreads();
-        }
-#pragma unroll
-        for (int cb = 0; cb < 4; ++cb) {
-            int colc = wv * 64 + cb * 16 + L;
+        f32x4 acch[2] = {{0.f,0.f,0.f,0.f},{0.f,0.f,0.f,0.f}};
+        for (int k = 0; k < 4; ++k) {
+            if (k < 3) stageWs(l1_wb + (size_t)(c * 256) * 256 + (k + 1) * 64, 256, cur ^ 1);
+            else       stageWs(l2_wb + c * 256, 1024, cur ^ 1);
+            mfma2(A1, k * 64, cur, acch);
+            __syncthreads();
+            cur ^= 1;
+        }
+#pragma unroll
+        for (int cb = 0; cb < 2; ++cb) {
+            int colc = wv * 32 + cb * 16 + L;
             float bv = l1b[c * 256 + colc];
 #pragma unroll
             for (int i = 0; i < 4; ++i)
                 hc[(rloc + i) * 264 + colc] = (ushort_t)f2bf1(fmaxf(acch[cb][i] + bv, 0.f));
         }
         __syncthreads();
-        for (int k0 = 0; k0 < 256; k0 += 64) {
-#pragma unroll
-            for (int j = 0; j < 8; ++j) {
-                int r0 = (wv * 8 + j) * 8;
-                const ushort_t* g = l2_wb + (size_t)(r0 + lrow) * 1024 + c * 256 + k0 + lchk;
-                stage_w16(g, &Ws[r0 * 64], ln);
-            }
-            __syncthreads();
-#pragma unroll
-            for (int kh = 0; kh < 2; ++kh) {
-                short8 af = *(const short8*)&hc[L * 264 + k0 + kh * 32 + quad * 8];
-#pragma unroll
-                for (int cb = 0; cb < 4; ++cb) {
-                    short8 bf = *(const short8*)&Ws[(wv * 64 + cb * 16 + L) * 64 + ((kh * 32 + quad * 8) ^ swz)];
-                    accf[cb] = __builtin_amdgcn_mfma_f32_16x16x32_bf16(af, bf, accf[cb], 0, 0, 0);
-                }
-            }
-            __syncthreads();
+        for (int k = 0; k < 4; ++k) {
+            if (k < 3)      stageWs(l2_wb + c * 256 + (k + 1) * 64, 1024, cur ^ 1);
+            else if (c < 3) stageWs(l1_wb + (size_t)((c + 1) * 256) * 256, 256, cur ^ 1);
+            mfma2(hc, k * 64, cur, accf);
+            __syncthreads();
+            cur ^= 1;
         }
     }
 
     {
         float s[4] = {0.f,0.f,0.f,0.f}, s2v[4] = {0.f,0.f,0.f,0.f};
 #pragma unroll
-        for (int cb = 0; cb < 4; ++cb) {
-            int col = wv * 64 + cb * 16 + L;
+        for (int cb = 0; cb < 2; ++cb) {
+            int col = wv * 32 + cb * 16 + L;
             float bv = l2b[col];
 #pragma unroll
             for (int i = 0; i < 4; ++i) {
@@ -853,15 +813,16 @@
         float mean[4], rstd[4];
 #pragma unroll
         for (int i = 0; i < 4; ++i) {
-            float St  = sS[0][rloc+i] + sS[1][rloc+i] + sS[2][rloc+i] + sS[3][rloc+i];
-            float S2t = s2S[0][rloc+i] + s2S[1][rloc+i] + s2S[2][rloc+i] + s2S[3][rloc+i];
+            float St = 0.f, S2t = 0.f;
+#pragma unroll
+            for (int w = 0; w < 8; ++w) { St += sS[w][rloc + i]; S2t += s2S[w][rloc + i]; }
             mean[i] = St * (1.f / 256.f);
             float var = S2t * (1.f / 256.f) - mean[i] * mean[i];
             rstd[i] = rsqrtf(var + 1e-5f);
         }
 #pragma unroll
-        for (int cb = 0; cb < 4; ++cb) {
-            int col = wv * 64 + cb * 16 + L;
+        for (int cb = 0; cb < 2; ++cb) {
+            int col = wv * 32 + cb * 16 + L;
             float gv = ln3g[col], bt = ln3b[col];
 #pragma unroll
             for (int i = 0; i < 4; ++i) {
@@ -908,6 +869,8 @@
     ushort_t* qkv16    = (ushort_t*)ws;
     ushort_t* att16    = (ushort_t*)(ws + 691200);
     float*    tgt_a    = ws + 1843200;
+    ushort_t* tgt16    = (ushort_t*)(ws + 1843200);
+    ushort_t* tq16     = (ushort_t*)(ws + 2310144);
     float*    px_g     = ws + 2995200;
     float*    py_g     = ws + 3456000;
     float*    aw_g     = ws + 3916800;
@@ -926,18 +889,19 @@
 
     dim3 b256(256);
 
-    hipLaunchKernelGGL(cvt_weights, dim3(496), b256, 0, stream,
-                       in_w, vp_w, outp_w, off_w, aw_w, op_w, l1w, l2w, wb);
+    hipLaunchKernelGGL(cvt_weights, dim3(1408), b256, 0, stream,
+                       in_w, vp_w, outp_w, off_w, aw_w, op_w, l1w, l2w, wb,
+                       tgt, qpos, tgt16, tq16);
     hipLaunchKernelGGL(proj_fused, dim3(1388), b256, 0, stream,
-                       tgt, qpos, in_wb, in_b, mem, vp_wb, vp_b, qkv16, value16);
+                       tq16, tgt16, in_wb, in_b, mem, vp_wb, vp_b, qkv16, value16);
     hipLaunchKernelGGL(sa_flash16, dim3(15, 32), b256, 0, stream, qkv16, att16);
-    hipLaunchKernelGGL(fused_ca, dim3(225), b256, 0, stream,
+    hipLaunchKernelGGL(fused_ca, dim3(225), dim3(512), 0, stream,
                        att16, tgt, qpos, outp_wb, outp_b, ln2g, ln2b,
                        off_wb, off_b, aw_wb, aw_b, refp,
                        tgt_a, px_g, py_g, aw_g);
     hipLaunchKernelGGL(msdeform4, dim3(900), b256, 0, stream,
                        px_g, py_g, aw_g, value16, att2_16);
-    hipLaunchKernelGGL(ffn_fused, dim3(225), b256, 0, stream,
+    hipLaunchKernelGGL(ffn_fused, dim3(225), dim3(512), 0, stream,
                        att2_16, tgt_a, op_wb, op_b, ln1g, ln1b,
                        l1_wb, l1b, l2_wb, l2b, ln3g, ln3b, out);
 }
```

Result: faster. 246.7 us (-3.3%).
